# Performance work log

Measured on AMD Instinct MI355X. Metric: run time of the kernel, lower is better.

## Reference

```python
import jax, jax.numpy as jnp
import numpy as np
import math

B, S, D, H = 2, 2048, 1024, 16
HD = D // H  # head_dim = 64

def setup_inputs() -> dict:
    key = jax.random.key(0)
    ks = jax.random.split(key, 11)
    def n(k, shape, scale=1.0):
        return jax.random.normal(k, shape, dtype=jnp.float32) * scale
    w_scale = 1.0 / math.sqrt(D)
    return {
        "q": n(ks[0], (B, S, D)),
        "k": n(ks[1], (B, S, D)),
        "v": n(ks[2], (B, S, D)),
        "WQ_w": n(ks[3], (D, D), w_scale),
        "WQ_b": n(ks[4], (D,), 0.01),
        "WK_w": n(ks[5], (D, D), w_scale),
        "WK_b": n(ks[6], (D,), 0.01),
        "WV_w": n(ks[7], (D, D), w_scale),
        "WV_b": n(ks[8], (D,), 0.01),
        "Wout_w": n(ks[9], (D, D), w_scale),
        "Wout_b": n(ks[10], (D,), 0.01),
    }

def reference(q, k, v, WQ_w, WQ_b, WK_w, WK_b, WV_w, WV_b, Wout_w, Wout_b):
    b, s, _ = k.shape
    # QKV projections (torch Linear: x @ W.T + b; here weights stored [in, out])
    qh = (q @ WQ_w + WQ_b).reshape(b, -1, H, HD).transpose(0, 2, 1, 3)  # [b,h,s,hd]
    kh = (k @ WK_w + WK_b).reshape(b, -1, H, HD).transpose(0, 2, 1, 3)
    vh = (v @ WV_w + WV_b).reshape(b, -1, H, HD).transpose(0, 2, 1, 3)
    # naive attention: full [b,h,s,s] score matrix
    scores = jnp.einsum("bhqd,bhkd->bhqk", qh, kh) / math.sqrt(HD)
    attn = jax.nn.softmax(scores, axis=-1)
    out = jnp.einsum("bhqk,bhkd->bhqd", attn, vh)
    concat = out.transpose(0, 2, 1, 3).reshape(b, -1, H * HD)  # [b,s,inner_dim]
    return concat @ Wout_w + Wout_b
```

## Files before the change

### kernel.cpp

```cpp
#include <hip/hip_runtime.h>
#include <hip/hip_bf16.h>
#include <stdint.h>

typedef __attribute__((ext_vector_type(8))) short bf16x8;
typedef __attribute__((ext_vector_type(4))) short short4v;
typedef __attribute__((ext_vector_type(4))) float f32x4;

#define MFMA16x16x32 __builtin_amdgcn_mfma_f32_16x16x32_bf16

__device__ __forceinline__ short f2b(float f) {
  union { float f; uint32_t u; } x;
  x.f = f;
  uint32_t u = x.u;
  uint32_t r = (u + 0x7FFFu + ((u >> 16) & 1u)) >> 16;
  return (short)(uint16_t)r;
}

__device__ __forceinline__ uint32_t cvt_pk_bf16(float lo, float hi) {
  uint32_t r;
  asm volatile("v_cvt_pk_bf16_f32 %0, %1, %2" : "=v"(r) : "v"(lo), "v"(hi));
  return r;
}
__device__ __forceinline__ float exp2_fast(float x) {
  float r;
  asm volatile("v_exp_f32 %0, %1" : "=v"(r) : "v"(x));
  return r;
}
__device__ __forceinline__ bf16x8 cvt8(const float4 a, const float4 b) {
  union { uint32_t u[4]; bf16x8 v; } o;
  o.u[0] = cvt_pk_bf16(a.x, a.y);
  o.u[1] = cvt_pk_bf16(a.z, a.w);
  o.u[2] = cvt_pk_bf16(b.x, b.y);
  o.u[3] = cvt_pk_bf16(b.z, b.w);
  return o.v;
}

__device__ __forceinline__ void async_copy16(const void* g, void* l) {
  __builtin_amdgcn_global_load_lds(
      (const __attribute__((address_space(1))) void*)g,
      (__attribute__((address_space(3))) void*)l, 16, 0, 0);
}

__global__ void prep_kernel(const float* __restrict__ W0,
                            const float* __restrict__ W1,
                            const float* __restrict__ W2,
                            const float* __restrict__ W3,
                            const float* __restrict__ q,
                            const float* __restrict__ k,
                            const float* __restrict__ v,
                            short* __restrict__ Wt,
                            short* __restrict__ xq,
                            short* __restrict__ xk,
                            short* __restrict__ xv) {
  __shared__ short tile[64][72];
  const int z = blockIdx.z;
  const int t = threadIdx.x;
  if (z < 4) {
    const float* W = (z == 0) ? W0 : (z == 1) ? W1 : (z == 2) ? W2 : W3;
    short* Wo = Wt + (size_t)z * 1024 * 1024;
    const int r0 = blockIdx.y * 64;
    const int c0 = blockIdx.x * 64;
#pragma unroll
    for (int i = 0; i < 4; ++i) {
      const int lin = i * 1024 + t * 4;
      const int r = lin >> 6, c = lin & 63;
      const float4 vv = *(const float4*)&W[(size_t)(r0 + r) * 1024 + c0 + c];
      tile[r][c + 0] = f2b(vv.x);
      tile[r][c + 1] = f2b(vv.y);
      tile[r][c + 2] = f2b(vv.z);
      tile[r][c + 3] = f2b(vv.w);
    }
    __syncthreads();
#pragma unroll
    for (int i = 0; i < 2; ++i) {
      const int lin = i * 2048 + t * 8;
      const int r = lin >> 6, c = lin & 63;
      bf16x8 ov;
#pragma unroll
      for (int jj = 0; jj < 8; ++jj) ov[jj] = tile[c + jj][r];
      *(bf16x8*)&Wo[(size_t)(c0 + r) * 1024 + r0 + c] = ov;
    }
  } else {
    const float* x = (z == 4) ? q : (z == 5) ? k : v;
    short* yp = (z == 4) ? xq : (z == 5) ? xk : xv;
    const int base = (blockIdx.y * 16 + blockIdx.x) * 256 + t;
#pragma unroll
    for (int j = 0; j < 8; ++j) {
      const int i = base + j * 65536;
      const float4 a = ((const float4*)x)[2 * i];
      const float4 b = ((const float4*)x)[2 * i + 1];
      ((bf16x8*)yp)[i] = cvt8(a, b);
    }
  }
}

__launch_bounds__(256, 2)
__global__ void gemm_qkv_kernel(const short* __restrict__ A0,
                                const short* __restrict__ A1,
                                const short* __restrict__ A2,
                                const short* __restrict__ WtBase,
                                const float* __restrict__ b0,
                                const float* __restrict__ b1,
                                const float* __restrict__ b2,
                                short* __restrict__ C0,
                                short* __restrict__ C1,
                                short* __restrict__ Vt,
                                int ybase) {
  const int K = 1024;
  __shared__ short As[128 * 64];
  __shared__ short Bs[128 * 64];

  const int y = blockIdx.y + ybase;
  const short* A = (y == 0) ? A0 : (y == 1) ? A1 : A2;
  const short* Wt = WtBase + (size_t)y * 1024 * 1024;
  const float* bias = (y == 0) ? b0 : (y == 1) ? b1 : b2;

  const int tm = blockIdx.x & 31;
  const int tn = blockIdx.x >> 5;
  const int m0 = tm * 128, n0 = tn * 128;

  const int tid = threadIdx.x;
  const int lane = tid & 63;
  const int w = tid >> 6;
  const int wr = w >> 1, wc = w & 1;
  const int hi = lane >> 4, cc = lane & 15;
  const int srow = lane >> 3, schunk = lane & 7;

  f32x4 acc[4][4] = {};

  for (int kt = 0; kt < 16; ++kt) {
    const int k0 = kt * 64;
#pragma unroll
    for (int i = 0; i < 4; ++i) {
      const int ri = w * 4 + i;
      const int row = ri * 8 + srow;
      const int gch = schunk ^ (row & 7);
      async_copy16(A + (size_t)(m0 + row) * K + (k0 + gch * 8), &As[ri * 512]);
      async_copy16(Wt + (size_t)(n0 + row) * K + (k0 + gch * 8), &Bs[ri * 512]);
    }
    __syncthreads();
#pragma unroll
    for (int kk = 0; kk < 2; ++kk) {
      bf16x8 af[4], bfr[4];
#pragma unroll
      for (int x = 0; x < 4; ++x) {
        const int gch = kk * 4 + hi;
        const int rowA = wr * 64 + x * 16 + cc;
        af[x] = *(const bf16x8*)&As[rowA * 64 + ((gch ^ (rowA & 7)) << 3)];
        const int rowB = wc * 64 + x * 16 + cc;
        bfr[x] = *(const bf16x8*)&Bs[rowB * 64 + ((gch ^ (rowB & 7)) << 3)];
      }
#pragma unroll
      for (int x = 0; x < 4; ++x)
#pragma unroll
        for (int yy = 0; yy < 4; ++yy)
          acc[x][yy] = MFMA16x16x32(af[x], bfr[yy], acc[x][yy], 0, 0, 0);
    }
    __syncthreads();
  }

  short* Cout = (y == 0) ? C0 : C1;
#pragma unroll
  for (int x = 0; x < 4; ++x) {
    const int rbase = m0 + wr * 64 + x * 16 + (hi << 2);
#pragma unroll
    for (int yy = 0; yy < 4; ++yy) {
      const int col = n0 + wc * 64 + yy * 16 + cc;
      const float bv = bias[col];
      if (y == 2) {
        const int b = rbase >> 11, s = rbase & 2047;
        const int hh = col >> 6, d = col & 63;
        short4v pack;
#pragma unroll
        for (int r = 0; r < 4; ++r) pack[r] = f2b(acc[x][yy][r] + bv);
        *(short4v*)&Vt[((size_t)(b * 16 + hh) * 64 + d) * 2048 + s] = pack;
      } else {
#pragma unroll
        for (int r = 0; r < 4; ++r)
          Cout[(size_t)(rbase + r) * 1024 + col] = f2b(acc[x][yy][r] + bv);
      }
    }
  }
}

__launch_bounds__(256, 2)
__global__ void gemm_out_kernel(const short* __restrict__ A,
                                const short* __restrict__ Wt,
                                const float* __restrict__ bias,
                                float* __restrict__ C) {
  const int N = 1024, K = 1024;
  __shared__ short As[128 * 64];
  __shared__ short Bs[128 * 64];

  const int tm = blockIdx.x & 31;
  const int tn = blockIdx.x >> 5;
  const int m0 = tm * 128, n0 = tn * 128;

  const int tid = threadIdx.x;
  const int lane = tid & 63;
  const int w = tid >> 6;
  const int wr = w >> 1, wc = w & 1;
  const int hi = lane >> 4, cc = lane & 15;
  const int srow = lane >> 3, schunk = lane & 7;

  f32x4 acc[4][4] = {};

  for (int kt = 0; kt < 16; ++kt) {
    const int k0 = kt * 64;
#pragma unroll
    for (int i = 0; i < 4; ++i) {
      const int ri = w * 4 + i;
      const int row = ri * 8 + srow;
      const int gch = schunk ^ (row & 7);
      async_copy16(A + (size_t)(m0 + row) * K + (k0 + gch * 8), &As[ri * 512]);
      async_copy16(Wt + (size_t)(n0 + row) * K + (k0 + gch * 8), &Bs[ri * 512]);
    }
    __syncthreads();
#pragma unroll
    for (int kk = 0; kk < 2; ++kk) {
      bf16x8 af[4], bfr[4];
#pragma unroll
      for (int x = 0; x < 4; ++x) {
        const int gch = kk * 4 + hi;
        const int rowA = wr * 64 + x * 16 + cc;
        af[x] = *(const bf16x8*)&As[rowA * 64 + ((gch ^ (rowA & 7)) << 3)];
        const int rowB = wc * 64 + x * 16 + cc;
        bfr[x] = *(const bf16x8*)&Bs[rowB * 64 + ((gch ^ (rowB & 7)) << 3)];
      }
#pragma unroll
      for (int x = 0; x < 4; ++x)
#pragma unroll
        for (int yy = 0; yy < 4; ++yy)
          acc[x][yy] = MFMA16x16x32(af[x], bfr[yy], acc[x][yy], 0, 0, 0);
    }
    __syncthreads();
  }

#pragma unroll
  for (int x = 0; x < 4; ++x) {
    const int rbase = m0 + wr * 64 + x * 16 + (hi << 2);
#pragma unroll
    for (int yy = 0; yy < 4; ++yy) {
      const int col = n0 + wc * 64 + yy * 16 + cc;
      const float bv = bias[col];
#pragma unroll
      for (int r = 0; r < 4; ++r)
        C[(size_t)(rbase + r) * N + col] = acc[x][yy][r] + bv;
    }
  }
}

__launch_bounds__(128, 2)
__global__ void attn_kernel(const short* __restrict__ qh,
                            const short* __restrict__ kh,
                            const short* __restrict__ Vt,
                            short* __restrict__ concat) {
  const int S = 2048;
  const float CL2 = 0.18033688011112042f;
  __shared__ short Ks[2][64 * 64];
  __shared__ short Vs[2][64 * 64];
  __shared__ short Ps[2][32 * 64];

  const int qb = blockIdx.x;
  const int h = blockIdx.y;
  const int b = blockIdx.z;
  const int tid = threadIdx.x, lane = tid & 63, w = tid >> 6;
  const int hi = lane >> 4, cc = lane & 15;

  const size_t rowbase = (size_t)b * S;
  const int q0 = qb * 64 + w * 32;

  bf16x8 qf[2][2];
#pragma unroll
  for (int aq = 0; aq < 2; ++aq)
#pragma unroll
    for (int kk = 0; kk < 2; ++kk) {
      const int col = h * 64 + kk * 32 + hi * 8;
      qf[aq][kk] =
          *(const bf16x8*)&qh[(rowbase + q0 + aq * 16 + cc) * 1024 + col];
    }

  f32x4 oacc[2][4] = {};
  float l[2] = {0.f, 0.f};

  const short* Vth = Vt + (size_t)(b * 16 + h) * 64 * 2048;
  short* Pw = &Ps[w][0];
  const int srow = lane >> 3, schunk = lane & 7;
  const int e0 = (cc >> 3) & 1;

#pragma unroll
  for (int i = 0; i < 4; ++i) {
    const int ri = w * 4 + i;
    const int row = ri * 8 + srow;
    const int gch = schunk ^ (row & 7);
    async_copy16(&kh[(rowbase + row) * 1024 + h * 64 + gch * 8], &Ks[0][ri * 512]);
    async_copy16(&Vth[(size_t)row * 2048 + gch * 8], &Vs[0][ri * 512]);
  }
  __syncthreads();

  for (int t = 0; t < S / 64; ++t) {
    const int cur = t & 1;
    if (t + 1 < S / 64) {
      const int kv0 = (t + 1) * 64;
#pragma unroll
      for (int i = 0; i < 4; ++i) {
        const int ri = w * 4 + i;
        const int row = ri * 8 + srow;
        const int gch = schunk ^ (row & 7);
        async_copy16(&kh[(rowbase + kv0 + row) * 1024 + h * 64 + gch * 8],
                     &Ks[cur ^ 1][ri * 512]);
        async_copy16(&Vth[(size_t)row * 2048 + kv0 + gch * 8],
                     &Vs[cur ^ 1][ri * 512]);
      }
    }

    f32x4 sacc[2][4] = {};
#pragma unroll
    for (int kk = 0; kk < 2; ++kk) {
      bf16x8 kf[4];
#pragma unroll
      for (int n = 0; n < 4; ++n) {
        const int row = n * 16 + cc;
        const int ch = (kk * 4 + hi) ^ (cc & 7);
        kf[n] = *(const bf16x8*)&Ks[cur][row * 64 + (ch << 3)];
      }
      __builtin_amdgcn_s_setprio(1);
#pragma unroll
      for (int aq = 0; aq < 2; ++aq)
#pragma unroll
        for (int n = 0; n < 4; ++n)
          sacc[aq][n] = MFMA16x16x32(kf[n], qf[aq][kk], sacc[aq][n], 0, 0, 0);
      __builtin_amdgcn_s_setprio(0);
    }

#pragma unroll
    for (int aq = 0; aq < 2; ++aq) {
      const int qrow = aq * 16 + cc;
#pragma unroll
      for (int n = 0; n < 4; ++n) {
        const float p0 = exp2_fast(sacc[aq][n][0] * CL2);
        const float p1 = exp2_fast(sacc[aq][n][1] * CL2);
        const float p2 = exp2_fast(sacc[aq][n][2] * CL2);
        const float p3 = exp2_fast(sacc[aq][n][3] * CL2);
        l[aq] += (p0 + p1) + (p2 + p3);
        const uint32_t u0 = cvt_pk_bf16(p0, p1);
        const uint32_t u1 = cvt_pk_bf16(p2, p3);
        const int chunk = (2 * n + (hi >> 1)) ^ (cc & 7);
        const int base = qrow * 64 + (chunk << 3) + ((hi & 1) << 2);
        *(uint32_t*)&Pw[base + (e0 << 1)] = e0 ? u1 : u0;
        *(uint32_t*)&Pw[base + ((e0 ^ 1) << 1)] = e0 ? u0 : u1;
      }
    }

#pragma unroll
    for (int kvh = 0; kvh < 2; ++kvh) {
      const int ch = (kvh * 4 + hi) ^ (cc & 7);
      bf16x8 pf[2], vf[4];
#pragma unroll
      for (int aq = 0; aq < 2; ++aq)
        pf[aq] = *(const bf16x8*)&Pw[(aq * 16 + cc) * 64 + (ch << 3)];
#pragma unroll
      for (int n = 0; n < 4; ++n) {
        const int row = n * 16 + cc;
        vf[n] = *(const bf16x8*)&Vs[cur][row * 64 + (ch << 3)];
      }
      __builtin_amdgcn_s_setprio(1);
#pragma unroll
      for (int aq = 0; aq < 2; ++aq)
#pragma unroll
        for (int n = 0; n < 4; ++n)
          oacc[aq][n] = MFMA16x16x32(vf[n], pf[aq], oacc[aq][n], 0, 0, 0);
      __builtin_amdgcn_s_setprio(0);
    }
    __syncthreads();
  }

#pragma unroll
  for (int aq = 0; aq < 2; ++aq) {
    float lv = l[aq];
    lv += __shfl_xor(lv, 16);
    lv += __shfl_xor(lv, 32);
    const float inv = 1.0f / lv;
    const size_t grow = rowbase + q0 + aq * 16 + cc;
#pragma unroll
    for (int n = 0; n < 4; ++n)
#pragma unroll
      for (int r = 0; r < 4; ++r) {
        const int d = n * 16 + hi * 4 + r;
        concat[grow * 1024 + h * 64 + d] = f2b(oacc[aq][n][r] * inv);
      }
  }
}

extern "C" void kernel_launch(void* const* d_in, const int* in_sizes, int n_in,
                              void* d_out, int out_size, void* d_ws, size_t ws_size,
                              hipStream_t stream) {
  const float* q = (const float*)d_in[0];
  const float* k = (const float*)d_in[1];
  const float* v = (const float*)d_in[2];
  const float* WQ = (const float*)d_in[3];
  const float* bQ = (const float*)d_in[4];
  const float* WK = (const float*)d_in[5];
  const float* bK = (const float*)d_in[6];
  const float* WV = (const float*)d_in[7];
  const float* bV = (const float*)d_in[8];
  const float* WO = (const float*)d_in[9];
  const float* bO = (const float*)d_in[10];

  char* ws = (char*)d_ws;
  const size_t MB = 1024 * 1024;
  short* Wt = (short*)ws;
  short* xq = (short*)(ws + 8 * MB);
  short* xk = (short*)(ws + 16 * MB);
  short* xv = (short*)(ws + 24 * MB);
  short* qh = (short*)(ws + 32 * MB);
  short* kh = (short*)(ws + 40 * MB);
  short* Vt = xq;
  short* concat = xk;

  prep_kernel<<<dim3(16, 16, 7), 256, 0, stream>>>(WQ, WK, WV, WO, q, k, v,
                                                   Wt, xq, xk, xv);
  gemm_qkv_kernel<<<dim3(256, 2), 256, 0, stream>>>(
      xq, xk, xv, Wt, bQ, bK, bV, qh, kh, Vt, 0);
  gemm_qkv_kernel<<<dim3(256, 1), 256, 0, stream>>>(
      xq, xk, xv, Wt, bQ, bK, bV, qh, kh, Vt, 2);
  attn_kernel<<<dim3(32, 16, 2), 128, 0, stream>>>(qh, kh, Vt, concat);
  gemm_out_kernel<<<256, 256, 0, stream>>>(concat, Wt + 3 * MB, bO,
                                           (float*)d_out);
}
```

Baseline: 138.5 us.

## Split attention over two KV halves with a separate weighted combine kernel

Adds a split-KV attention kernel. Each block handles 128 query rows with 4 waves over one half of the 2048 keys and writes a partial normalized output plus its row sums. A combine kernel then merges the two halves, weighting each by its share of the row sum. Blocks grow to 256 threads, so each K/V tile staged in shared memory is reused by twice as many query rows. The softmax-to-PV step is also interleaved per query subtile, with V fragments loaded up front. The cost is an extra kernel launch, extra global traffic for the partial outputs, and a second bf16 rounding of the output; the fallback attention kernel is reshaped to 256 threads and drops its setprio hints.

```diff
diff --git a/kernel.cpp b/kernel.cpp
--- a/kernel.cpp
+++ b/kernel.cpp
@@ -14,6 +14,11 @@
   uint32_t u = x.u;
   uint32_t r = (u + 0x7FFFu + ((u >> 16) & 1u)) >> 16;
   return (short)(uint16_t)r;
+}
+__device__ __forceinline__ float b2f(short s) {
+  union { float f; uint32_t u; } x;
+  x.u = ((uint32_t)(uint16_t)s) << 16;
+  return x.f;
 }
 
 __device__ __forceinline__ uint32_t cvt_pk_bf16(float lo, float hi) {
@@ -250,7 +255,172 @@
   }
 }
 
-__launch_bounds__(128, 2)
+__launch_bounds__(256, 4)
+__global__ void attn_split_kernel(const short* __restrict__ qh,
+                                  const short* __restrict__ kh,
+                                  const short* __restrict__ Vt,
+                                  short* __restrict__ O0,
+                                  short* __restrict__ O1,
+                                  float* __restrict__ lbuf) {
+  const float CL2 = 0.18033688011112042f;
+  __shared__ short Ks[2][64 * 64];
+  __shared__ short Vs[2][64 * 64];
+  __shared__ short Ps[4][16 * 64];
+
+  const int qb = blockIdx.x;
+  const int h = blockIdx.y;
+  const int b = blockIdx.z >> 1;
+  const int half = blockIdx.z & 1;
+  const int tid = threadIdx.x, lane = tid & 63, w = tid >> 6;
+  const int hi = lane >> 4, cc = lane & 15;
+
+  const size_t rowbase = (size_t)b * 2048;
+  const int q0 = qb * 128 + w * 32;
+  const int kvbase = half * 1024;
+  short* O = half ? O1 : O0;
+
+  bf16x8 qf[2][2];
+#pragma unroll
+  for (int aq = 0; aq < 2; ++aq)
+#pragma unroll
+    for (int kk = 0; kk < 2; ++kk) {
+      const int col = h * 64 + kk * 32 + hi * 8;
+      qf[aq][kk] =
+          *(const bf16x8*)&qh[(rowbase + q0 + aq * 16 + cc) * 1024 + col];
+    }
+
+  f32x4 oacc[2][4] = {};
+  float l[2] = {0.f, 0.f};
+
+  const short* Vth = Vt + (size_t)(b * 16 + h) * 64 * 2048;
+  short* Pw = &Ps[w][0];
+  const int srow = lane >> 3, schunk = lane & 7;
+  const int e0 = (cc >> 3) & 1;
+
+#pragma unroll
+  for (int i = 0; i < 2; ++i) {
+    const int ri = w * 2 + i;
+    const int row = ri * 8 + srow;
+    const int gch = schunk ^ (row & 7);
+    async_copy16(&kh[(rowbase + kvbase + row) * 1024 + h * 64 + gch * 8],
+                 &Ks[0][ri * 512]);
+    async_copy16(&Vth[(size_t)row * 2048 + kvbase + gch * 8], &Vs[0][ri * 512]);
+  }
+  __syncthreads();
+
+  for (int t = 0; t < 16; ++t) {
+    const int cur = t & 1;
+    if (t + 1 < 16) {
+      const int kv0 = kvbase + (t + 1) * 64;
+#pragma unroll
+      for (int i = 0; i < 2; ++i) {
+        const int ri = w * 2 + i;
+        const int row = ri * 8 + srow;
+        const int gch = schunk ^ (row & 7);
+        async_copy16(&kh[(rowbase + kv0 + row) * 1024 + h * 64 + gch * 8],
+                     &Ks[cur ^ 1][ri * 512]);
+        async_copy16(&Vth[(size_t)row * 2048 + kv0 + gch * 8],
+                     &Vs[cur ^ 1][ri * 512]);
+      }
+    }
+
+    f32x4 sacc[2][4] = {};
+#pragma unroll
+    for (int kk = 0; kk < 2; ++kk) {
+      bf16x8 kf[4];
+#pragma unroll
+      for (int n = 0; n < 4; ++n) {
+        const int row = n * 16 + cc;
+        const int ch = (kk * 4 + hi) ^ (cc & 7);
+        kf[n] = *(const bf16x8*)&Ks[cur][row * 64 + (ch << 3)];
+      }
+      __builtin_amdgcn_s_setprio(1);
+#pragma unroll
+      for (int aq = 0; aq < 2; ++aq)
+#pragma unroll
+        for (int n = 0; n < 4; ++n)
+          sacc[aq][n] = MFMA16x16x32(kf[n], qf[aq][kk], sacc[aq][n], 0, 0, 0);
+      __builtin_amdgcn_s_setprio(0);
+    }
+
+    bf16x8 vf[2][4];
+#pragma unroll
+    for (int kvh = 0; kvh < 2; ++kvh) {
+      const int ch = (kvh * 4 + hi) ^ (cc & 7);
+#pragma unroll
+      for (int n = 0; n < 4; ++n)
+        vf[kvh][n] = *(const bf16x8*)&Vs[cur][(n * 16 + cc) * 64 + (ch << 3)];
+    }
+
+#pragma unroll
+    for (int aq = 0; aq < 2; ++aq) {
+#pragma unroll
+      for (int n = 0; n < 4; ++n) {
+        const float p0 = exp2_fast(sacc[aq][n][0] * CL2);
+        const float p1 = exp2_fast(sacc[aq][n][1] * CL2);
+        const float p2 = exp2_fast(sacc[aq][n][2] * CL2);
+        const float p3 = exp2_fast(sacc[aq][n][3] * CL2);
+        l[aq] += (p0 + p1) + (p2 + p3);
+        const uint32_t u0 = cvt_pk_bf16(p0, p1);
+        const uint32_t u1 = cvt_pk_bf16(p2, p3);
+        const int chunk = (2 * n + (hi >> 1)) ^ (cc & 7);
+        const int base = cc * 64 + (chunk << 3) + ((hi & 1) << 2);
+        *(uint32_t*)&Pw[base + (e0 << 1)] = e0 ? u1 : u0;
+        *(uint32_t*)&Pw[base + ((e0 ^ 1) << 1)] = e0 ? u0 : u1;
+      }
+#pragma unroll
+      for (int kvh = 0; kvh < 2; ++kvh) {
+        const int ch = (kvh * 4 + hi) ^ (cc & 7);
+        const bf16x8 pf = *(const bf16x8*)&Pw[cc * 64 + (ch << 3)];
+        __builtin_amdgcn_s_setprio(1);
+#pragma unroll
+        for (int n = 0; n < 4; ++n)
+          oacc[aq][n] = MFMA16x16x32(vf[kvh][n], pf, oacc[aq][n], 0, 0, 0);
+        __builtin_amdgcn_s_setprio(0);
+      }
+    }
+    __syncthreads();
+  }
+
+#pragma unroll
+  for (int aq = 0; aq < 2; ++aq) {
+    float lv = l[aq];
+    lv += __shfl_xor(lv, 16);
+    lv += __shfl_xor(lv, 32);
+    const float inv = 1.0f / lv;
+    const size_t grow = rowbase + q0 + aq * 16 + cc;
+#pragma unroll
+    for (int n = 0; n < 4; ++n)
+#pragma unroll
+      for (int r = 0; r < 4; ++r) {
+        const int d = n * 16 + hi * 4 + r;
+        O[grow * 1024 + h * 64 + d] = f2b(oacc[aq][n][r] * inv);
+      }
+    if (hi == 0) lbuf[(half << 16) + grow * 16 + h] = lv;
+  }
+}
+
+__global__ void combine_kernel(const short* __restrict__ O0,
+                               const short* __restrict__ O1,
+                               const float* __restrict__ lbuf,
+                               short* __restrict__ out) {
+  const int i = blockIdx.x * 256 + threadIdx.x;
+  const int row = i >> 7;
+  const int h = (i & 127) >> 3;
+  const float l0 = lbuf[row * 16 + h];
+  const float l1 = lbuf[65536 + row * 16 + h];
+  const float inv = 1.0f / (l0 + l1);
+  const float w0 = l0 * inv, w1 = l1 * inv;
+  const bf16x8 a = ((const bf16x8*)O0)[i];
+  const bf16x8 b = ((const bf16x8*)O1)[i];
+  bf16x8 o;
+#pragma unroll
+  for (int j = 0; j < 8; ++j)
+    o[j] = f2b(w0 * b2f(a[j]) + w1 * b2f(b[j]));
+  ((bf16x8*)out)[i] = o;
+}
+
+__launch_bounds__(256, 2)
 __global__ void attn_kernel(const short* __restrict__ qh,
                             const short* __restrict__ kh,
                             const short* __restrict__ Vt,
@@ -259,7 +429,7 @@
   const float CL2 = 0.18033688011112042f;
   __shared__ short Ks[2][64 * 64];
   __shared__ short Vs[2][64 * 64];
-  __shared__ short Ps[2][32 * 64];
+  __shared__ short Ps[4 * 32 * 64];
 
   const int qb = blockIdx.x;
   const int h = blockIdx.y;
@@ -268,7 +438,7 @@
   const int hi = lane >> 4, cc = lane & 15;
 
   const size_t rowbase = (size_t)b * S;
-  const int q0 = qb * 64 + w * 32;
+  const int q0 = qb * 128 + w * 32;
 
   bf16x8 qf[2][2];
 #pragma unroll
@@ -284,13 +454,13 @@
   float l[2] = {0.f, 0.f};
 
   const short* Vth = Vt + (size_t)(b * 16 + h) * 64 * 2048;
-  short* Pw = &Ps[w][0];
+  short* Pw = &Ps[w * 2048];
   const int srow = lane >> 3, schunk = lane & 7;
   const int e0 = (cc >> 3) & 1;
 
 #pragma unroll
-  for (int i = 0; i < 4; ++i) {
-    const int ri = w * 4 + i;
+  for (int i = 0; i < 2; ++i) {
+    const int ri = w * 2 + i;
     const int row = ri * 8 + srow;
     const int gch = schunk ^ (row & 7);
     async_copy16(&kh[(rowbase + row) * 1024 + h * 64 + gch * 8], &Ks[0][ri * 512]);
@@ -303,8 +473,8 @@
     if (t + 1 < S / 64) {
       const int kv0 = (t + 1) * 64;
 #pragma unroll
-      for (int i = 0; i < 4; ++i) {
-        const int ri = w * 4 + i;
+      for (int i = 0; i < 2; ++i) {
+        const int ri = w * 2 + i;
         const int row = ri * 8 + srow;
         const int gch = schunk ^ (row & 7);
         async_copy16(&kh[(rowbase + kv0 + row) * 1024 + h * 64 + gch * 8],
@@ -324,13 +494,11 @@
         const int ch = (kk * 4 + hi) ^ (cc & 7);
         kf[n] = *(const bf16x8*)&Ks[cur][row * 64 + (ch << 3)];
       }
-      __builtin_amdgcn_s_setprio(1);
 #pragma unroll
       for (int aq = 0; aq < 2; ++aq)
 #pragma unroll
         for (int n = 0; n < 4; ++n)
           sacc[aq][n] = MFMA16x16x32(kf[n], qf[aq][kk], sacc[aq][n], 0, 0, 0);
-      __builtin_amdgcn_s_setprio(0);
     }
 
 #pragma unroll
@@ -364,13 +532,11 @@
         const int row = n * 16 + cc;
         vf[n] = *(const bf16x8*)&Vs[cur][row * 64 + (ch << 3)];
       }
-      __builtin_amdgcn_s_setprio(1);
 #pragma unroll
       for (int aq = 0; aq < 2; ++aq)
 #pragma unroll
         for (int n = 0; n < 4; ++n)
           oacc[aq][n] = MFMA16x16x32(vf[n], pf[aq], oacc[aq][n], 0, 0, 0);
-      __builtin_amdgcn_s_setprio(0);
     }
     __syncthreads();
   }
@@ -415,6 +581,7 @@
   short* xv = (short*)(ws + 24 * MB);
   short* qh = (short*)(ws + 32 * MB);
   short* kh = (short*)(ws + 40 * MB);
+  float* lbuf = (float*)(ws + 48 * MB);
   short* Vt = xq;
   short* concat = xk;
 
@@ -424,7 +591,15 @@
       xq, xk, xv, Wt, bQ, bK, bV, qh, kh, Vt, 0);
   gemm_qkv_kernel<<<dim3(256, 1), 256, 0, stream>>>(
       xq, xk, xv, Wt, bQ, bK, bV, qh, kh, Vt, 2);
-  attn_kernel<<<dim3(32, 16, 2), 128, 0, stream>>>(qh, kh, Vt, concat);
+
+  if (ws_size >= 49 * MB) {
+    attn_split_kernel<<<dim3(16, 16, 4), 256, 0, stream>>>(
+        qh, kh, Vt, concat, xv, lbuf);
+    combine_kernel<<<2048, 256, 0, stream>>>(concat, xv, lbuf, concat);
+  } else {
+    attn_kernel<<<dim3(16, 16, 2), 256, 0, stream>>>(qh, kh, Vt, concat);
+  }
+
   gemm_out_kernel<<<256, 256, 0, stream>>>(concat, Wt + 3 * MB, bO,
                                            (float*)d_out);
 }
```

After: 210.0 us. 51.6% more time.
